# Kernel tuning notes

Measured on AMD Instinct MI355X. Metric: run time of the kernel, lower is better.

Reference implementation:

```python
import jax, jax.numpy as jnp
import numpy as np

R = 16
ALPHA = 32
SCALING = ALPHA / R  # 2.0


def setup_inputs() -> dict:
    key = jax.random.key(0)
    k_x, k_w, k_b, k_a, k_bm = jax.random.split(key, 5)
    d = 1024
    x = jax.random.normal(k_x, (4, 4096, d), dtype=jnp.float32)
    W = jax.random.normal(k_w, (d, d), dtype=jnp.float32) * 0.02
    b = jax.random.normal(k_b, (d,), dtype=jnp.float32) * 0.02
    A = jax.random.normal(k_a, (R, d), dtype=jnp.float32) * 0.02
    B = jax.random.normal(k_bm, (d, R), dtype=jnp.float32) * 0.02
    return {"x": x, "W": W, "b": b, "A": A, "B": B}


def reference(x, W, b, A, B):
    # base linear: x @ W^T + b   (W: [out, in])
    base = jnp.einsum("bsd,od->bso", x, W) + b
    # low-rank update: (x @ A^T) @ B^T, scaled (dropout p=0 -> identity)
    u = jnp.einsum("bsd,rd->bsr", x, A)   # [B, S, r]
    update = jnp.einsum("bsr,or->bso", u, B)
    return base + SCALING * update
```

## Files before the change

kernel.cpp:

```cpp
#include <hip/hip_runtime.h>


typedef __bf16 bf16x8 __attribute__((ext_vector_type(8)));
typedef float f32x4 __attribute__((ext_vector_type(4)));
typedef unsigned short ushort8 __attribute__((ext_vector_type(8)));

__device__ __forceinline__ unsigned short f2bf(float f) {
    __bf16 h = (__bf16)f;
    union { __bf16 b; unsigned short u; } v; v.b = h; return v.u;
}
__device__ __forceinline__ ushort8 cvt8(f32x4 a, f32x4 b) {
    ushort8 o;
#pragma unroll
    for (int i = 0; i < 4; ++i) { o[i] = f2bf(a[i]); o[i + 4] = f2bf(b[i]); }
    return o;
}
__device__ __forceinline__ void gld16(const unsigned short* g, unsigned short* l) {
    __builtin_amdgcn_global_load_lds(
        (const __attribute__((address_space(1))) unsigned int*)g,
        (__attribute__((address_space(3))) unsigned int*)l, 16, 0, 0);
}

#define FENCE() asm volatile("" ::: "memory")
#define BARRIER() do { FENCE(); __builtin_amdgcn_s_barrier(); FENCE(); } while (0)

__global__ __launch_bounds__(256) void prep(
    const float* __restrict__ X, const float* __restrict__ W,
    const float* __restrict__ A, const float* __restrict__ B,
    unsigned short* __restrict__ xbf, unsigned short* __restrict__ Weff)
{
    const int b = blockIdx.x;
    if (b < 512) {
        const int idx = b * 256 + threadIdx.x;
        const int o  = idx >> 7;
        const int kc = (idx & 127) << 3;
        float br[16];
#pragma unroll
        for (int r = 0; r < 16; ++r) br[r] = 2.0f * B[o * 16 + r];
        float acc[8];
        const float* wrow = W + (size_t)o * 1024 + kc;
#pragma unroll
        for (int j = 0; j < 8; ++j) acc[j] = wrow[j];
#pragma unroll
        for (int r = 0; r < 16; ++r) {
            const float* arow = A + r * 1024 + kc;
#pragma unroll
            for (int j = 0; j < 8; ++j) acc[j] += br[r] * arow[j];
        }
        ushort8 o8;
#pragma unroll
        for (int j = 0; j < 8; ++j) o8[j] = f2bf(acc[j]);
        *(ushort8*)(Weff + (size_t)o * 1024 + kc) = o8;
    } else {
        const size_t i = ((size_t)(b - 512) * 256 + threadIdx.x) * 8;
        f32x4 a = *(const f32x4*)(X + i);
        f32x4 c = *(const f32x4*)(X + i + 4);
        *(ushort8*)(xbf + i) = cvt8(a, c);
    }
}

#define PHASE_MFMA(LO)                                              \
    do { BARRIER();                                                 \
         asm volatile("s_waitcnt lgkmcnt(0)" ::: "memory");         \
         __builtin_amdgcn_sched_barrier(0);            \
         __builtin_amdgcn_s_setprio(1);                             \
         _Pragma("unroll")                                          \
         for (int m2 = 0; m2 < 4; ++m2)                             \
             _Pragma("unroll")                                      \
             for (int n2 = 0; n2 < 2; ++n2)                         \
                 acc[(LO) + m2][n2] = __builtin_amdgcn_mfma_f32_16x16x32_bf16( \
                     fa[(LO) + m2], fb[n2], acc[(LO) + m2][n2], 0, 0, 0);      \
         __builtin_amdgcn_s_setprio(0);                             \
         BARRIER(); } while (0)

__global__ __launch_bounds__(512, 4) void gemm256(
    const unsigned short* __restrict__ Xb,
    const unsigned short* __restrict__ Wt,
    const float* __restrict__ bias,
    float* __restrict__ out)
{
    extern __shared__ __align__(16) unsigned short lds[];

    const int t    = threadIdx.x;
    const int lane = t & 63;
    const int w    = t >> 6;
    const int wr   = w >> 2;
    const int wc   = w & 3;
    const int r16  = lane & 15;
    const int quad = lane >> 4;

    const int nwg = gridDim.x;
    int swz = blockIdx.x;
    if ((nwg & 7) == 0) swz = (swz & 7) * (nwg >> 3) + (swz >> 3);
    const int bm = (swz >> 3) * 256;
    const int bn = (swz & 7) * 128;

    const int r  = t >> 2;
    const int sc = (t & 3) ^ (r & 3);
    const unsigned short* pA0 = Xb + (size_t)(bm + r) * 1024 + sc * 8;
    const unsigned short* pA1 = pA0 + 131072;
    const unsigned short* pB  = Wt + (size_t)(bn + r) * 1024 + sc * 8;
    const int lc = t * 8;

    const int sw = (quad ^ (r16 & 3)) * 8;
    const int aB = wr * 512 + r16 * 32 + sw;
    const int bB = wc * 512 + r16 * 32 + sw;

    f32x4 acc[8][2];
#pragma unroll
    for (int i = 0; i < 8; ++i)
#pragma unroll
        for (int jj = 0; jj < 2; ++jj)
            acc[i][jj] = (f32x4){0.f, 0.f, 0.f, 0.f};

    gld16(pA0,      lds + lc);                 FENCE();
    gld16(pB,       lds + 8192 + lc);          FENCE();
    gld16(pA1,      lds + 4096 + lc);          FENCE();
    gld16(pA0 + 32, lds + 12288 + lc);         FENCE();
    gld16(pB  + 32, lds + 12288 + 8192 + lc);
    asm volatile("s_waitcnt vmcnt(2)" ::: "memory");
    BARRIER();

#pragma unroll 2
    for (int j = 0; j < 32; ++j) {
        const int cur  = (j & 1) * 12288;
        const int next = cur ^ 12288;
        const unsigned short* Lb = lds + cur;
        const int k1 = (j + 1) * 32, k2 = (j + 2) * 32;

        bf16x8 fa[8], fb[2];

#pragma unroll
        for (int mt = 0; mt < 4; ++mt)
            fa[mt] = *(const bf16x8*)(Lb + mt * 1024 + aB);
#pragma unroll
        for (int nt = 0; nt < 2; ++nt)
            fb[nt] = *(const bf16x8*)(Lb + 8192 + nt * 2048 + bB);
        if (j < 31) gld16(pA1 + k1, lds + next + 4096 + lc);
        PHASE_MFMA(0);

#pragma unroll
        for (int mt = 4; mt < 8; ++mt)
            fa[mt] = *(const bf16x8*)(Lb + 4096 + (mt - 4) * 1024 + aB);
        if (j < 30) { gld16(pA0 + k2, lds + cur + lc);              FENCE();
                      gld16(pB  + k2, lds + cur + 8192 + lc); }
        if (j < 30)       asm volatile("s_waitcnt vmcnt(2)" ::: "memory");
        else if (j == 30) asm volatile("s_waitcnt vmcnt(0)" ::: "memory");
        PHASE_MFMA(4);
    }

    const int orow0 = bm + wr * 16 + quad * 4;
    const int ocol0 = bn + wc * 16 + r16;
#pragma unroll
    for (int nt = 0; nt < 2; ++nt) {
        const float bv = bias[ocol0 + nt * 64];
#pragma unroll
        for (int mt = 0; mt < 8; ++mt) {
            float* orow = out + (size_t)(orow0 + mt * 32) * 1024 + (ocol0 + nt * 64);
#pragma unroll
            for (int i = 0; i < 4; ++i)
                orow[(size_t)i * 1024] = acc[mt][nt][i] + bv;
        }
    }
}

template <bool XF32>
__global__ __launch_bounds__(256) void gemm_bt(
    const void* __restrict__ X_, const unsigned short* __restrict__ Wt,
    const float* __restrict__ bias, float* __restrict__ out)
{
    __shared__ __align__(16) unsigned short lA[128 * 32];
    __shared__ __align__(16) unsigned short lB[128 * 32];

    const int t    = threadIdx.x;
    const int lane = t & 63;
    const int w    = t >> 6;
    const int bm   = blockIdx.x * 128;
    const int bn   = blockIdx.y * 128;
    const int wm   = (w & 1) * 64;
    const int wn   = (w >> 1) * 64;
    const int r16  = lane & 15;
    const int quad = lane >> 4;

    const int srow = t >> 2;
    const int gc   = (t & 3) ^ ((srow >> 1) & 3);
    unsigned short* lsA = lA + t * 8;
    unsigned short* lsB = lB + t * 8;
    const size_t ga0 = (size_t)(bm + srow) * 1024 + gc * 8;
    const size_t ga1 = (size_t)(bm + srow + 64) * 1024 + gc * 8;
    const unsigned short* gB0 = Wt + (size_t)(bn + srow) * 1024 + gc * 8;

    const int p    = (quad ^ ((r16 >> 1) & 3)) * 8;
    const int aoff = (wm + r16) * 32 + p;
    const int boff = (wn + r16) * 32 + p;

    const unsigned short* Xb = (const unsigned short*)X_;
    const float*          Xf = (const float*)X_;

    f32x4 acc[4][4];
#pragma unroll
    for (int i = 0; i < 4; ++i)
#pragma unroll
        for (int j = 0; j < 4; ++j) {
            f32x4 z = {0.f, 0.f, 0.f, 0.f};
            acc[i][j] = z;
        }

    for (int kt = 0; kt < 1024; kt += 32) {
        if (XF32) {
            f32x4 a0 = *(const f32x4*)(Xf + ga0 + kt);
            f32x4 a1 = *(const f32x4*)(Xf + ga0 + kt + 4);
            f32x4 a2 = *(const f32x4*)(Xf + ga1 + kt);
            f32x4 a3 = *(const f32x4*)(Xf + ga1 + kt + 4);
            *(ushort8*)lsA          = cvt8(a0, a1);
            *(ushort8*)(lsA + 2048) = cvt8(a2, a3);
        } else {
            gld16(Xb + ga0 + kt, lsA);
            gld16(Xb + ga1 + kt, lsA + 2048);
        }
        gld16(gB0 + kt,             lsB);
        gld16(gB0 + kt + 64 * 1024, lsB + 2048);
        __syncthreads();

        bf16x8 fa[4], fb[4];
#pragma unroll
        for (int mt = 0; mt < 4; ++mt) fa[mt] = *(const bf16x8*)(lA + aoff + mt * 16 * 32);
#pragma unroll
        for (int nt = 0; nt < 4; ++nt) fb[nt] = *(const bf16x8*)(lB + boff + nt * 16 * 32);

#pragma unroll
        for (int mt = 0; mt < 4; ++mt)
#pragma unroll
            for (int nt = 0; nt < 4; ++nt)
                acc[mt][nt] = __builtin_amdgcn_mfma_f32_16x16x32_bf16(
                    fa[mt], fb[nt], acc[mt][nt], 0, 0, 0);

        __syncthreads();
    }

    const int orow0 = bm + wm + quad * 4;
    const int ocol0 = bn + wn + r16;
#pragma unroll
    for (int nt = 0; nt < 4; ++nt) {
        const float bv = bias[ocol0 + nt * 16];
#pragma unroll
        for (int mt = 0; mt < 4; ++mt)
#pragma unroll
            for (int i = 0; i < 4; ++i)
                out[(size_t)(orow0 + mt * 16 + i) * 1024 + (ocol0 + nt * 16)] =
                    acc[mt][nt][i] + bv;
    }
}

extern "C" void kernel_launch(void* const* d_in, const int* in_sizes, int n_in,
                              void* d_out, int out_size, void* d_ws, size_t ws_size,
                              hipStream_t stream) {
    const float* x  = (const float*)d_in[0];
    const float* W  = (const float*)d_in[1];
    const float* b  = (const float*)d_in[2];
    const float* A  = (const float*)d_in[3];
    const float* Bm = (const float*)d_in[4];
    float* out = (float*)d_out;

    const int M = in_sizes[0] / 1024;

    const bool fast = (ws_size >= ((size_t)(M)*1024*2 + (2u << 20) + 4096)) &&
                      (M % 256 == 0);
    if (fast) {
        unsigned short* xbf  = (unsigned short*)d_ws;
        unsigned short* Weff = xbf + (size_t)M * 1024;
        hipLaunchKernelGGL(prep, dim3(512 + M / 2), dim3(256), 0, stream,
                           x, W, A, Bm, xbf, Weff);
        hipLaunchKernelGGL(gemm256, dim3((M / 256) * 8), dim3(512), 49152, stream,
                           xbf, Weff, b, out);
    } else {
        unsigned short* Weff = (unsigned short*)d_ws;
        hipLaunchKernelGGL(prep, dim3(512), dim3(256), 0, stream,
                           x, W, A, Bm, (unsigned short*)nullptr, Weff);
        hipLaunchKernelGGL((gemm_bt<true>), dim3(M / 128, 8), dim3(256), 0, stream,
                           (const void*)x, Weff, b, out);
    }
}
```

Baseline: 155.6 us.

## Fuse fp32-to-bf16 conversion of x into GEMM tile loading

Removes the separate prep pass that converted all activations to bf16 in a workspace. The GEMM now loads fp32 x into registers, converts to bf16 and stores into swizzled LDS, while W still uses direct global-to-LDS loads. This eliminates an extra write and read of the bf16 activation copy. In exchange, each column-tile block re-reads fp32 activations, doubling A-side global traffic, and adds VALU conversion and register pressure to the main loop.

```diff
diff --git a/kernel.cpp b/kernel.cpp
--- a/kernel.cpp
+++ b/kernel.cpp
@@ -25,38 +25,29 @@
 #define BARRIER() do { FENCE(); __builtin_amdgcn_s_barrier(); FENCE(); } while (0)
 
 __global__ __launch_bounds__(256) void prep(
-    const float* __restrict__ X, const float* __restrict__ W,
-    const float* __restrict__ A, const float* __restrict__ B,
-    unsigned short* __restrict__ xbf, unsigned short* __restrict__ Weff)
+    const float* __restrict__ W, const float* __restrict__ A,
+    const float* __restrict__ B, unsigned short* __restrict__ Weff)
 {
-    const int b = blockIdx.x;
-    if (b < 512) {
-        const int idx = b * 256 + threadIdx.x;
-        const int o  = idx >> 7;
-        const int kc = (idx & 127) << 3;
-        float br[16];
-#pragma unroll
-        for (int r = 0; r < 16; ++r) br[r] = 2.0f * B[o * 16 + r];
-        float acc[8];
-        const float* wrow = W + (size_t)o * 1024 + kc;
-#pragma unroll
-        for (int j = 0; j < 8; ++j) acc[j] = wrow[j];
-#pragma unroll
-        for (int r = 0; r < 16; ++r) {
-            const float* arow = A + r * 1024 + kc;
-#pragma unroll
-            for (int j = 0; j < 8; ++j) acc[j] += br[r] * arow[j];
-        }
-        ushort8 o8;
-#pragma unroll
-        for (int j = 0; j < 8; ++j) o8[j] = f2bf(acc[j]);
-        *(ushort8*)(Weff + (size_t)o * 1024 + kc) = o8;
-    } else {
-        const size_t i = ((size_t)(b - 512) * 256 + threadIdx.x) * 8;
-        f32x4 a = *(const f32x4*)(X + i);
-        f32x4 c = *(const f32x4*)(X + i + 4);
-        *(ushort8*)(xbf + i) = cvt8(a, c);
-    }
+    const int idx = blockIdx.x * 256 + threadIdx.x;
+    const int o  = idx >> 7;
+    const int kc = (idx & 127) << 3;
+    float br[16];
+#pragma unroll
+    for (int r = 0; r < 16; ++r) br[r] = 2.0f * B[o * 16 + r];
+    float acc[8];
+    const float* wrow = W + (size_t)o * 1024 + kc;
+#pragma unroll
+    for (int j = 0; j < 8; ++j) acc[j] = wrow[j];
+#pragma unroll
+    for (int r = 0; r < 16; ++r) {
+        const float* arow = A + r * 1024 + kc;
+#pragma unroll
+        for (int j = 0; j < 8; ++j) acc[j] += br[r] * arow[j];
+    }
+    ushort8 o8;
+#pragma unroll
+    for (int j = 0; j < 8; ++j) o8[j] = f2bf(acc[j]);
+    *(ushort8*)(Weff + (size_t)o * 1024 + kc) = o8;
 }
 
 #define PHASE_MFMA(LO)                                              \
@@ -74,7 +65,7 @@
          BARRIER(); } while (0)
 
 __global__ __launch_bounds__(512, 4) void gemm256(
-    const unsigned short* __restrict__ Xb,
+    const float* __restrict__ Xf,
     const unsigned short* __restrict__ Wt,
     const float* __restrict__ bias,
     float* __restrict__ out)
@@ -96,13 +87,15 @@
     const int bn = (swz & 7) * 128;
 
     const int r  = t >> 2;
-    const int sc = (t & 3) ^ (r & 3);
-    const unsigned short* pA0 = Xb + (size_t)(bm + r) * 1024 + sc * 8;
-    const unsigned short* pA1 = pA0 + 131072;
-    const unsigned short* pB  = Wt + (size_t)(bn + r) * 1024 + sc * 8;
+    const int c  = t & 3;
+    const int xr = c ^ ((r >> 1) & 3);
+    const float* gA0 = Xf + (size_t)(bm + r) * 1024 + c * 8;
+    const float* gA1 = gA0 + 131072;
+    const unsigned short* pB = Wt + (size_t)(bn + r) * 1024 + xr * 8;
+    const int wd = r * 32 + xr * 8;
     const int lc = t * 8;
 
-    const int sw = (quad ^ (r16 & 3)) * 8;
+    const int sw = (quad ^ ((r16 >> 1) & 3)) * 8;
     const int aB = wr * 512 + r16 * 32 + sw;
     const int bB = wc * 512 + r16 * 32 + sw;
 
@@ -113,38 +106,54 @@
         for (int jj = 0; jj < 2; ++jj)
             acc[i][jj] = (f32x4){0.f, 0.f, 0.f, 0.f};
 
-    gld16(pA0,      lds + lc);                 FENCE();
-    gld16(pB,       lds + 8192 + lc);          FENCE();
-    gld16(pA1,      lds + 4096 + lc);          FENCE();
-    gld16(pA0 + 32, lds + 12288 + lc);         FENCE();
-    gld16(pB  + 32, lds + 12288 + 8192 + lc);
-    asm volatile("s_waitcnt vmcnt(2)" ::: "memory");
+    f32x4 sA[4];
+
+    sA[0] = *(const f32x4*)(gA0);      sA[1] = *(const f32x4*)(gA0 + 4);
+    sA[2] = *(const f32x4*)(gA1);      sA[3] = *(const f32x4*)(gA1 + 4);
+    FENCE();
+    gld16(pB, lds + 8192 + lc);        FENCE();
+    *(ushort8*)(lds + wd)        = cvt8(sA[0], sA[1]);
+    *(ushort8*)(lds + 4096 + wd) = cvt8(sA[2], sA[3]);
+    sA[0] = *(const f32x4*)(gA0 + 32); sA[1] = *(const f32x4*)(gA0 + 36);
+    sA[2] = *(const f32x4*)(gA1 + 32); sA[3] = *(const f32x4*)(gA1 + 36);
+    FENCE();
+    gld16(pB + 32, lds + 12288 + 8192 + lc);
+    asm volatile("s_waitcnt vmcnt(5)" ::: "memory");
+    asm volatile("s_waitcnt lgkmcnt(0)" ::: "memory");
     BARRIER();
 
 #pragma unroll 2
     for (int j = 0; j < 32; ++j) {
-        const int cur  = (j & 1) * 12288;
-        const int next = cur ^ 12288;
+        const int cur = (j & 1) * 12288;
+        const int nxt = cur ^ 12288;
         const unsigned short* Lb = lds + cur;
-        const int k1 = (j + 1) * 32, k2 = (j + 2) * 32;
+        const int k2 = (j + 2) * 32;
 
         bf16x8 fa[8], fb[2];
 
+        if (j < 31) {
+            *(ushort8*)(lds + nxt + wd)        = cvt8(sA[0], sA[1]);
+            *(ushort8*)(lds + nxt + 4096 + wd) = cvt8(sA[2], sA[3]);
+        }
 #pragma unroll
         for (int mt = 0; mt < 4; ++mt)
             fa[mt] = *(const bf16x8*)(Lb + mt * 1024 + aB);
 #pragma unroll
         for (int nt = 0; nt < 2; ++nt)
             fb[nt] = *(const bf16x8*)(Lb + 8192 + nt * 2048 + bB);
-        if (j < 31) gld16(pA1 + k1, lds + next + 4096 + lc);
         PHASE_MFMA(0);
 
 #pragma unroll
         for (int mt = 4; mt < 8; ++mt)
             fa[mt] = *(const bf16x8*)(Lb + 4096 + (mt - 4) * 1024 + aB);
-        if (j < 30) { gld16(pA0 + k2, lds + cur + lc);              FENCE();
-                      gld16(pB  + k2, lds + cur + 8192 + lc); }
-        if (j < 30)       asm volatile("s_waitcnt vmcnt(2)" ::: "memory");
+        if (j < 30) {
+            sA[0] = *(const f32x4*)(gA0 + k2);      sA[1] = *(const f32x4*)(gA0 + k2 + 4);
+            sA[2] = *(const f32x4*)(gA1 + k2);      sA[3] = *(const f32x4*)(gA1 + k2 + 4);
+            FENCE();
+            gld16(pB + k2, lds + cur + 8192 + lc);
+            FENCE();
+        }
+        if (j < 30)       asm volatile("s_waitcnt vmcnt(5)" ::: "memory");
         else if (j == 30) asm volatile("s_waitcnt vmcnt(0)" ::: "memory");
         PHASE_MFMA(4);
     }
@@ -264,19 +273,13 @@
 
     const int M = in_sizes[0] / 1024;
 
-    const bool fast = (ws_size >= ((size_t)(M)*1024*2 + (2u << 20) + 4096)) &&
-                      (M % 256 == 0);
+    const bool fast = (ws_size >= (2u << 20) + 4096) && (M % 256 == 0);
+    unsigned short* Weff = (unsigned short*)d_ws;
+    hipLaunchKernelGGL(prep, dim3(512), dim3(256), 0, stream, W, A, Bm, Weff);
     if (fast) {
-        unsigned short* xbf  = (unsigned short*)d_ws;
-        unsigned short* Weff = xbf + (size_t)M * 1024;
-        hipLaunchKernelGGL(prep, dim3(512 + M / 2), dim3(256), 0, stream,
-                           x, W, A, Bm, xbf, Weff);
         hipLaunchKernelGGL(gemm256, dim3((M / 256) * 8), dim3(512), 49152, stream,
-                           xbf, Weff, b, out);
+                           x, Weff, b, out);
     } else {
-        unsigned short* Weff = (unsigned short*)d_ws;
-        hipLaunchKernelGGL(prep, dim3(512), dim3(256), 0, stream,
-                           x, W, A, Bm, (unsigned short*)nullptr, Weff);
         hipLaunchKernelGGL((gemm_bt<true>), dim3(M / 128, 8), dim3(256), 0, stream,
                            (const void*)x, Weff, b, out);
     }
```

Result: slower. 179.7 us (+15.5%).
